# Kernel optimization log

Hardware: AMD Instinct MI355X
Metric: run time of the kernel (lower is better)

## Reference

```python
import jax, jax.numpy as jnp
import numpy as np

B, T0, H0, W0 = 8, 32, 16, 16
DV, DA, NH = 1024, 512, 16
L2 = 2048
EPS = 1e-6


def setup_inputs() -> dict:
    key = jax.random.key(0)
    ks = jax.random.split(key, 16)
    s = 0.02
    inp = {
        "video_x": jax.random.normal(ks[0], (B, T0 * H0 * W0, DV), jnp.float32),
        "audio_x": jax.random.normal(ks[1], (B, L2, DA), jnp.float32),
        "probe": jax.random.normal(ks[2], (1, 1, DV), jnp.float32) * s,
        "wq": jax.random.normal(ks[3], (DV, DV), jnp.float32) * s,
        "wk": jax.random.normal(ks[4], (DV, DV), jnp.float32) * s,
        "wv": jax.random.normal(ks[5], (DV, DV), jnp.float32) * s,
        "bq": jnp.zeros((DV,), jnp.float32),
        "bk": jnp.zeros((DV,), jnp.float32),
        "bv": jnp.zeros((DV,), jnp.float32),
        "wo": jax.random.normal(ks[6], (DV, DV), jnp.float32) * s,
        "bo": jnp.zeros((DV,), jnp.float32),
        "ln_g": jnp.ones((DV,), jnp.float32),
        "ln_b": jnp.zeros((DV,), jnp.float32),
        "proj_w": jax.random.normal(ks[7], (DA, DV), jnp.float32) * s,
        "proj_b": jnp.zeros((DA,), jnp.float32),
        "logit_scale": jnp.array([3.0], jnp.float32),
        "logit_bias": jnp.array([-3.9], jnp.float32),
        "T": T0, "H": H0, "W": W0,
    }
    return inp


def reference(video_x, audio_x, probe, wq, wk, wv, bq, bk, bv, wo, bo,
              ln_g, ln_b, proj_w, proj_b, logit_scale, logit_bias, T, H, W):
    Bv, L1, D = video_x.shape
    S = H * W
    dh = D // NH
    x = video_x.reshape(Bv, T, S, D)
    # single probe query, shared across B*T: project once
    q = (probe[0, 0] @ wq.T + bq).reshape(NH, dh)                      # [h,dh]
    k = (jnp.einsum('btsd,ed->btse', x, wk) + bk).reshape(Bv, T, S, NH, dh)
    v = (jnp.einsum('btsd,ed->btse', x, wv) + bv).reshape(Bv, T, S, NH, dh)
    scores = jnp.einsum('hd,btshd->bthcaptured'[:0] or 0, k) if False else jnp.einsum('hd,btshd->btsh', q, k) / jnp.sqrt(jnp.float32(dh))
    attn = jax.nn.softmax(scores, axis=2)                              # over S
    ctx = jnp.einsum('btsh,btshd->bthd', attn, v).reshape(Bv, T, D)
    pooled = ctx @ wo.T + bo                                           # [B,T,D]
    # LayerNorm
    mu = pooled.mean(-1, keepdims=True)
    var = ((pooled - mu) ** 2).mean(-1, keepdims=True)
    pooled = (pooled - mu) / jnp.sqrt(var + EPS) * ln_g + ln_b
    # project to audio dim, L2-normalize both sides
    vt = pooled @ proj_w.T + proj_b                                    # [B,T,Da]
    vt = vt / jnp.linalg.norm(vt, axis=-1, keepdims=True)
    a = audio_x / jnp.linalg.norm(audio_x, axis=-1, keepdims=True)
    sim = jnp.einsum('btd,bld->btl', vt, a)
    return sim * jnp.exp(logit_scale[0]) + logit_bias[0]
```

## Files before the change

kernel.cpp:

```cpp
#include <hip/hip_runtime.h>


#define FB_QWT    0u
#define FB_QB     16384u
#define FB_QF     16400u
#define FB_CTXX   18432u
#define FB_CTXP   4212736u
#define FB_POOLP  4737024u
#define FB_LNO    5261312u
#define FB_VTP    5523456u
#define FB_FLOATS 5785600u

typedef __attribute__((ext_vector_type(8))) short short8v;
typedef __attribute__((ext_vector_type(4))) float float4v;

__device__ __forceinline__ void bar_lds() {
    asm volatile("s_waitcnt lgkmcnt(0)\n\ts_barrier" ::: "memory");
}

__global__ __launch_bounds__(256) void k_qflat(const float* __restrict__ probe,
                                               const float* __restrict__ wq,
                                               const float* __restrict__ bq,
                                               float* __restrict__ qf) {
    int e = blockIdx.x, tid = threadIdx.x;
    const float* wr = wq + (size_t)e * 1024;
    float s = 0.f;
    for (int k = tid; k < 1024; k += 256) s += probe[k] * wr[k];
    s += __shfl_xor(s, 1);  s += __shfl_xor(s, 2);  s += __shfl_xor(s, 4);
    s += __shfl_xor(s, 8);  s += __shfl_xor(s, 16); s += __shfl_xor(s, 32);
    __shared__ float sm[4];
    if ((tid & 63) == 0) sm[tid >> 6] = s;
    __syncthreads();
    if (tid == 0) qf[e] = sm[0] + sm[1] + sm[2] + sm[3] + bq[e];
}

__global__ __launch_bounds__(64) void k_qwt(const float* __restrict__ qf,
                                            const float* __restrict__ wk,
                                            const float* __restrict__ bk,
                                            float* __restrict__ qwt_hd,
                                            float* __restrict__ qbs) {
    int kc = blockIdx.x, h = blockIdx.y, tid = threadIdx.x;
    int d = kc * 64 + tid;
    float s = 0.f;
    for (int e0 = 0; e0 < 64; ++e0) {
        int e = h * 64 + e0;
        s += qf[e] * wk[(size_t)e * 1024 + d];
    }
    qwt_hd[h * 1024 + d] = s * 0.125f;
    if (kc == 0) {
        float p = qf[h * 64 + tid] * bk[h * 64 + tid];
        p += __shfl_xor(p, 1);  p += __shfl_xor(p, 2);  p += __shfl_xor(p, 4);
        p += __shfl_xor(p, 8);  p += __shfl_xor(p, 16); p += __shfl_xor(p, 32);
        if (tid == 0) qbs[h] = p * 0.125f;
    }
}

__device__ __forceinline__ unsigned bf_rne(float f) {
    unsigned u = __float_as_uint(f);
    return (u + 0x7FFFu + ((u >> 16) & 1u)) >> 16;
}
__device__ __forceinline__ uint2 pack_bf4(float4 v) {
    uint2 r;
    r.x = bf_rne(v.x) | (bf_rne(v.y) << 16);
    r.y = bf_rne(v.z) | (bf_rne(v.w) << 16);
    return r;
}

__global__ __launch_bounds__(512, 2) void k1_attn(const float* __restrict__ x,
                                                  const float* __restrict__ qwt_hd,
                                                  const float* __restrict__ qbs,
                                                  float* __restrict__ ctxx) {
    __shared__ __align__(16) unsigned short xbf[16][1056];
    __shared__ __align__(16) unsigned short qwbf[16][1056];
    __shared__ __align__(16) float part[8][16][16];
    __shared__ __align__(16) float p_lds[16][16];
    __shared__ float qb_lds[16];
    __shared__ float linv_lds[16];

    const int tid  = threadIdx.x;
    const int lane = tid & 63;
    const int w    = tid >> 6;
    const int hq   = tid >> 7;
    const int cc   = tid & 127;
    const int bt   = blockIdx.x;
    const float* xb = x + (size_t)bt * 262144;

#pragma unroll
    for (int i = 0; i < 8; ++i) {
        int f4i = tid + i * 512;
        int hr = f4i >> 8, col4 = f4i & 255;
        float4 v = *(const float4*)(qwt_hd + hr * 1024 + col4 * 4);
        *(uint2*)&qwbf[hr][col4 * 4] = pack_bf4(v);
    }
    if (tid < 16) qb_lds[tid] = qbs[tid];

    float lacc = 0.f;
    float4 acc[8];
#pragma unroll
    for (int i = 0; i < 8; ++i) acc[i] = make_float4(0.f, 0.f, 0.f, 0.f);

    float4 st[8];
#pragma unroll
    for (int i = 0; i < 8; ++i)
        st[i] = *(const float4*)(xb + (size_t)(tid + i * 512) * 4);

    for (int c = 0; c < 16; ++c) {
        bar_lds();
#pragma unroll
        for (int i = 0; i < 8; ++i) {
            int f4i = tid + i * 512;
            int r = f4i >> 8, col4 = f4i & 255;
            *(uint2*)&xbf[r][col4 * 4] = pack_bf4(st[i]);
        }
        if (c < 15) {
            const float* nb = xb + (size_t)(c + 1) * 16384;
#pragma unroll
            for (int i = 0; i < 8; ++i)
                st[i] = *(const float4*)(nb + (size_t)(tid + i * 512) * 4);
        }
        bar_lds();
        {
            const int row = lane & 15;
            const int g   = lane >> 4;
            float4v cfr = {0.f, 0.f, 0.f, 0.f};
#pragma unroll
            for (int ks = 0; ks < 4; ++ks) {
                const int koff = (w * 4 + ks) * 32 + g * 8;
                short8v afr = *(const short8v*)&xbf[row][koff];
                short8v bfr = *(const short8v*)&qwbf[row][koff];
                cfr = __builtin_amdgcn_mfma_f32_16x16x32_bf16(afr, bfr, cfr, 0, 0, 0);
            }
#pragma unroll
            for (int r2 = 0; r2 < 4; ++r2)
                part[w][(lane >> 4) * 4 + r2][lane & 15] = cfr[r2];
        }
        bar_lds();
        if (tid < 256) {
            int s = tid >> 4, h = tid & 15;
            float sc = 0.f;
#pragma unroll
            for (int pw = 0; pw < 8; ++pw) sc += part[pw][s][h];
            p_lds[s][h] = __expf(sc + qb_lds[h]);
        }
        bar_lds();
        if (tid < 16) {
            float ll = 0.f;
#pragma unroll
            for (int s = 0; s < 16; ++s) ll += p_lds[s][tid];
            lacc += ll;
        }
#pragma unroll
        for (int r = 0; r < 16; ++r) {
            uint4 xv = *(const uint4*)&xbf[r][cc * 8];
            float x0 = __uint_as_float(xv.x << 16);
            float x1 = __uint_as_float(xv.x & 0xFFFF0000u);
            float x2 = __uint_as_float(xv.y << 16);
            float x3 = __uint_as_float(xv.y & 0xFFFF0000u);
            float x4 = __uint_as_float(xv.z << 16);
            float x5 = __uint_as_float(xv.z & 0xFFFF0000u);
            float x6 = __uint_as_float(xv.w << 16);
            float x7 = __uint_as_float(xv.w & 0xFFFF0000u);
            float4 p4 = *(const float4*)&p_lds[r][hq * 4];
            acc[0].x += p4.x * x0; acc[0].y += p4.x * x1; acc[0].z += p4.x * x2; acc[0].w += p4.x * x3;
            acc[1].x += p4.y * x0; acc[1].y += p4.y * x1; acc[1].z += p4.y * x2; acc[1].w += p4.y * x3;
            acc[2].x += p4.z * x0; acc[2].y += p4.z * x1; acc[2].z += p4.z * x2; acc[2].w += p4.z * x3;
            acc[3].x += p4.w * x0; acc[3].y += p4.w * x1; acc[3].z += p4.w * x2; acc[3].w += p4.w * x3;
            acc[4].x += p4.x * x4; acc[4].y += p4.x * x5; acc[4].z += p4.x * x6; acc[4].w += p4.x * x7;
            acc[5].x += p4.y * x4; acc[5].y += p4.y * x5; acc[5].z += p4.y * x6; acc[5].w += p4.y * x7;
            acc[6].x += p4.z * x4; acc[6].y += p4.z * x5; acc[6].z += p4.z * x6; acc[6].w += p4.z * x7;
            acc[7].x += p4.w * x4; acc[7].y += p4.w * x5; acc[7].z += p4.w * x6; acc[7].w += p4.w * x7;
        }
    }

    bar_lds();
    if (tid < 16) linv_lds[tid] = 1.0f / lacc;
    bar_lds();
    float* ob = ctxx + (size_t)bt * 16384;
#pragma unroll
    for (int i = 0; i < 4; ++i) {
        float li = linv_lds[hq * 4 + i];
        float4 o0 = acc[i];
        float4 o1 = acc[4 + i];
        o0.x *= li; o0.y *= li; o0.z *= li; o0.w *= li;
        o1.x *= li; o1.y *= li; o1.z *= li; o1.w *= li;
        float* dst = ob + (hq * 4 + i) * 1024 + cc * 8;
        *(float4*)dst = o0;
        *(float4*)(dst + 4) = o1;
    }
}

template<int FOLD>
__global__ __launch_bounds__(256, 2) void k_gemm2(const float* __restrict__ A0,
                                                  const float* __restrict__ A1,
                                                  const float* __restrict__ biask,
                                                  const float* __restrict__ Bw,
                                                  float* __restrict__ outp,
                                                  unsigned a_rstride, unsigned a_cstride,
                                                  unsigned ostride) {
    __shared__ __align__(16) float a_s[16][68];
    __shared__ __align__(16) float b_s[64][68];
    const int tid = threadIdx.x;
    const int rc = blockIdx.x;
    const int cb = blockIdx.y;
    const int ks = blockIdx.z;
    const int koff = ks * 512;
    const int rr = tid >> 4;
    const int ee = tid & 15;

    const size_t abase = (size_t)(rc * 16 + rr) * a_rstride + (size_t)cb * a_cstride + koff;

    float ac0 = 0.f, ac1 = 0.f, ac2 = 0.f, ac3 = 0.f;

    for (int kc = 0; kc < 8; ++kc) {
        __syncthreads();
        {
            float4 av = *(const float4*)(A0 + abase + kc * 64 + ee * 4);
            if (FOLD == 1) {
                float4 a1v = *(const float4*)(A1 + abase + kc * 64 + ee * 4);
                float4 bk4 = *(const float4*)(biask + koff + kc * 64 + ee * 4);
                av.x += a1v.x + bk4.x; av.y += a1v.y + bk4.y;
                av.z += a1v.z + bk4.z; av.w += a1v.w + bk4.w;
            }
            *(float4*)&a_s[rr][ee * 4] = av;
        }
#pragma unroll
        for (int i = 0; i < 4; ++i) {
            int f4i = tid + i * 256;
            int e = f4i >> 4, k4 = f4i & 15;
            float4 bv4 = *(const float4*)(Bw + (size_t)(cb * 64 + e) * 1024 + koff + kc * 64 + k4 * 4);
            int cs = (k4 + (e >> 2)) & 15;
            *(float4*)&b_s[e][cs * 4] = bv4;
        }
        __syncthreads();
#pragma unroll
        for (int k4 = 0; k4 < 16; ++k4) {
            float4 av = *(const float4*)&a_s[rr][k4 * 4];
            int cs = (k4 + ee) & 15;
            float4 b0 = *(const float4*)&b_s[ee * 4 + 0][cs * 4];
            float4 b1 = *(const float4*)&b_s[ee * 4 + 1][cs * 4];
            float4 b2 = *(const float4*)&b_s[ee * 4 + 2][cs * 4];
            float4 b3 = *(const float4*)&b_s[ee * 4 + 3][cs * 4];
            ac0 += av.x * b0.x + av.y * b0.y + av.z * b0.z + av.w * b0.w;
            ac1 += av.x * b1.x + av.y * b1.y + av.z * b1.z + av.w * b1.w;
            ac2 += av.x * b2.x + av.y * b2.y + av.z * b2.z + av.w * b2.w;
            ac3 += av.x * b3.x + av.y * b3.y + av.z * b3.z + av.w * b3.w;
        }
    }
    float4 o = make_float4(ac0, ac1, ac2, ac3);
    *(float4*)(outp + (size_t)ks * 256 * ostride + (size_t)(rc * 16 + rr) * ostride + cb * 64 + ee * 4) = o;
}

__global__ __launch_bounds__(256) void k_ln(const float* __restrict__ poolp,
                                            const float* __restrict__ bo,
                                            const float* __restrict__ g,
                                            const float* __restrict__ bb,
                                            float* __restrict__ out) {
    __shared__ float sm[8];
    int row = blockIdx.x, tid = threadIdx.x;
    float4 v0 = *(const float4*)(poolp + (size_t)row * 1024 + tid * 4);
    float4 v1 = *(const float4*)(poolp + 262144u + (size_t)row * 1024 + tid * 4);
    float4 bv = *(const float4*)(bo + tid * 4);
    float4 v;
    v.x = v0.x + v1.x + bv.x; v.y = v0.y + v1.y + bv.y;
    v.z = v0.z + v1.z + bv.z; v.w = v0.w + v1.w + bv.w;
    float s = v.x + v.y + v.z + v.w;
    float q = v.x * v.x + v.y * v.y + v.z * v.z + v.w * v.w;
    s += __shfl_xor(s, 1);  q += __shfl_xor(q, 1);
    s += __shfl_xor(s, 2);  q += __shfl_xor(q, 2);
    s += __shfl_xor(s, 4);  q += __shfl_xor(q, 4);
    s += __shfl_xor(s, 8);  q += __shfl_xor(q, 8);
    s += __shfl_xor(s, 16); q += __shfl_xor(q, 16);
    s += __shfl_xor(s, 32); q += __shfl_xor(q, 32);
    if ((tid & 63) == 0) { sm[tid >> 6] = s; sm[4 + (tid >> 6)] = q; }
    __syncthreads();
    float S = sm[0] + sm[1] + sm[2] + sm[3];
    float Q = sm[4] + sm[5] + sm[6] + sm[7];
    float mu = S * (1.f / 1024.f);
    float var = Q * (1.f / 1024.f) - mu * mu;
    float rs = rsqrtf(var + 1e-6f);
    float4 gg = *(const float4*)(g + tid * 4);
    float4 be = *(const float4*)(bb + tid * 4);
    float4 o;
    o.x = (v.x - mu) * rs * gg.x + be.x;
    o.y = (v.y - mu) * rs * gg.y + be.y;
    o.z = (v.z - mu) * rs * gg.z + be.z;
    o.w = (v.w - mu) * rs * gg.w + be.w;
    *(float4*)(out + (size_t)row * 1024 + tid * 4) = o;
}

__global__ __launch_bounds__(256, 2) void k_sim(const float* __restrict__ vtp,
                                                const float* __restrict__ pb,
                                                const float* __restrict__ audio,
                                                const float* __restrict__ ls,
                                                const float* __restrict__ lb,
                                                float* __restrict__ out) {
    __shared__ float a_s[64][65];
    __shared__ float v_s[32][65];
    __shared__ float rinv_a[64];
    __shared__ float rinv_v[32];
    const int tid = threadIdx.x;
    const int lc = blockIdx.x;
    const int b  = blockIdx.y;
    const int al = tid >> 2, ak = (tid & 3) * 16;
    const int vl = tid >> 3, vk = (tid & 7) * 8;
    const int rg = tid >> 4, lg = tid & 15;
    float ssa = 0.f, ssv = 0.f;
    float c00=0,c01=0,c02=0,c03=0,c10=0,c11=0,c12=0,c13=0;

    for (int kc = 0; kc < 8; ++kc) {
        __syncthreads();
        {
            const float* ap = audio + (size_t)b * 1048576 + (size_t)(lc * 64 + al) * 512 + kc * 64 + ak;
#pragma unroll
            for (int i = 0; i < 4; ++i) {
                float4 wv4 = *(const float4*)(ap + i * 4);
                ssa += wv4.x * wv4.x + wv4.y * wv4.y + wv4.z * wv4.z + wv4.w * wv4.w;
                a_s[al][ak + i * 4 + 0] = wv4.x; a_s[al][ak + i * 4 + 1] = wv4.y;
                a_s[al][ak + i * 4 + 2] = wv4.z; a_s[al][ak + i * 4 + 3] = wv4.w;
            }
            const size_t voff = (size_t)(b * 32 + vl) * 512 + kc * 64 + vk;
#pragma unroll
            for (int i = 0; i < 2; ++i) {
                float4 p0 = *(const float4*)(vtp + voff + i * 4);
                float4 p1 = *(const float4*)(vtp + 131072u + voff + i * 4);
                float4 pbv = *(const float4*)(pb + kc * 64 + vk + i * 4);
                float4 wv4;
                wv4.x = p0.x + p1.x + pbv.x; wv4.y = p0.y + p1.y + pbv.y;
                wv4.z = p0.z + p1.z + pbv.z; wv4.w = p0.w + p1.w + pbv.w;
                ssv += wv4.x * wv4.x + wv4.y * wv4.y + wv4.z * wv4.z + wv4.w * wv4.w;
                v_s[vl][vk + i * 4 + 0] = wv4.x; v_s[vl][vk + i * 4 + 1] = wv4.y;
                v_s[vl][vk + i * 4 + 2] = wv4.z; v_s[vl][vk + i * 4 + 3] = wv4.w;
            }
        }
        __syncthreads();
#pragma unroll 2
        for (int k = 0; k < 64; ++k) {
            float v0 = v_s[rg * 2 + 0][k];
            float v1 = v_s[rg * 2 + 1][k];
            float x0 = a_s[lg * 4 + 0][k];
            float x1 = a_s[lg * 4 + 1][k];
            float x2 = a_s[lg * 4 + 2][k];
            float x3 = a_s[lg * 4 + 3][k];
            c00 += v0 * x0; c01 += v0 * x1; c02 += v0 * x2; c03 += v0 * x3;
            c10 += v1 * x0; c11 += v1 * x1; c12 += v1 * x2; c13 += v1 * x3;
        }
    }
    ssa += __shfl_xor(ssa, 1); ssa += __shfl_xor(ssa, 2);
    if ((tid & 3) == 0) rinv_a[al] = rsqrtf(ssa);
    ssv += __shfl_xor(ssv, 1); ssv += __shfl_xor(ssv, 2); ssv += __shfl_xor(ssv, 4);
    if ((tid & 7) == 0) rinv_v[vl] = rsqrtf(ssv);
    __syncthreads();
    const float sc = __expf(ls[0]);
    const float bias = lb[0];
    float ra0 = rinv_a[lg * 4 + 0], ra1 = rinv_a[lg * 4 + 1];
    float ra2 = rinv_a[lg * 4 + 2], ra3 = rinv_a[lg * 4 + 3];
    float accs[2][4] = {{c00,c01,c02,c03},{c10,c11,c12,c13}};
#pragma unroll
    for (int cr = 0; cr < 2; ++cr) {
        int t = rg * 2 + cr;
        float rv = rinv_v[t] * sc;
        float4 o;
        o.x = accs[cr][0] * rv * ra0 + bias;
        o.y = accs[cr][1] * rv * ra1 + bias;
        o.z = accs[cr][2] * rv * ra2 + bias;
        o.w = accs[cr][3] * rv * ra3 + bias;
        *(float4*)(out + (size_t)b * 65536 + (size_t)t * 2048 + lc * 64 + lg * 4) = o;
    }
}

extern "C" void kernel_launch(void* const* d_in, const int* in_sizes, int n_in,
                              void* d_out, int out_size, void* d_ws, size_t ws_size,
                              hipStream_t stream) {
    (void)in_sizes; (void)n_in; (void)out_size;
    const float* video = (const float*)d_in[0];
    const float* audio = (const float*)d_in[1];
    const float* probe = (const float*)d_in[2];
    const float* wq    = (const float*)d_in[3];
    const float* wk    = (const float*)d_in[4];
    const float* wv    = (const float*)d_in[5];
    const float* bq    = (const float*)d_in[6];
    const float* bk    = (const float*)d_in[7];
    const float* bv    = (const float*)d_in[8];
    const float* wo    = (const float*)d_in[9];
    const float* bo    = (const float*)d_in[10];
    const float* lng   = (const float*)d_in[11];
    const float* lnb   = (const float*)d_in[12];
    const float* pw    = (const float*)d_in[13];
    const float* pb    = (const float*)d_in[14];
    const float* ls    = (const float*)d_in[15];
    const float* lb    = (const float*)d_in[16];
    float* ws  = (float*)d_ws;
    float* out = (float*)d_out;
    if (ws_size < FB_FLOATS * sizeof(float)) return;

    float* qwt  = ws + FB_QWT;
    float* qbs  = ws + FB_QB;
    float* qf   = ws + FB_QF;
    float* ctxx = ws + FB_CTXX;
    float* ctxp = ws + FB_CTXP;
    float* poolp= ws + FB_POOLP;
    float* lno  = ws + FB_LNO;
    float* vtp  = ws + FB_VTP;

    k_qflat<<<dim3(1024), dim3(256), 0, stream>>>(probe, wq, bq, qf);
    k_qwt<<<dim3(16, 16), dim3(64), 0, stream>>>(qf, wk, bk, qwt, qbs);
    k1_attn<<<dim3(256), dim3(512), 0, stream>>>(video, qwt, qbs, ctxx);
    k_gemm2<0><<<dim3(16, 16, 2), dim3(256), 0, stream>>>(ctxx, nullptr, nullptr, wv, ctxp,
                                                          16384u, 1024u, 1024u);
    k_gemm2<1><<<dim3(16, 16, 2), dim3(256), 0, stream>>>(ctxp, ctxp + 262144u, bv, wo, poolp,
                                                          1024u, 0u, 1024u);
    k_ln<<<dim3(256), dim3(256), 0, stream>>>(poolp, bo, lng, lnb, lno);
    k_gemm2<0><<<dim3(16, 8, 2), dim3(256), 0, stream>>>(lno, nullptr, nullptr, pw, vtp,
                                                         1024u, 0u, 512u);
    k_sim<<<dim3(32, 8), dim3(256), 0, stream>>>(vtp, pb, audio, ls, lb, out);
}
```

Before: 173.4 us.

## Fuse query prep kernels, swizzle LDS tiles, store context in bf16

Merges the two probe-query preparation kernels into a single 16-block kernel that keeps the projected query in shared memory, removing one launch and a global round trip. Applies an XOR swizzle to the bf16 x and query tiles in LDS to cut bank conflicts on the MFMA fragment and context reads. Writes the attention context as bf16 instead of fp32 and has the next GEMM read bf16, halving that intermediate traffic at the cost of extra rounding. The fused prep kernel runs on only 16 blocks, which may leave it latency bound.

```diff
diff --git a/kernel.cpp b/kernel.cpp
--- a/kernel.cpp
+++ b/kernel.cpp
@@ -18,37 +18,42 @@
     asm volatile("s_waitcnt lgkmcnt(0)\n\ts_barrier" ::: "memory");
 }
 
-__global__ __launch_bounds__(256) void k_qflat(const float* __restrict__ probe,
+#define SW(R, C) ((C) ^ (((R) & 7) << 3))
+
+__global__ __launch_bounds__(256) void k_qprep(const float* __restrict__ probe,
                                                const float* __restrict__ wq,
                                                const float* __restrict__ bq,
-                                               float* __restrict__ qf) {
-    int e = blockIdx.x, tid = threadIdx.x;
-    const float* wr = wq + (size_t)e * 1024;
-    float s = 0.f;
-    for (int k = tid; k < 1024; k += 256) s += probe[k] * wr[k];
-    s += __shfl_xor(s, 1);  s += __shfl_xor(s, 2);  s += __shfl_xor(s, 4);
-    s += __shfl_xor(s, 8);  s += __shfl_xor(s, 16); s += __shfl_xor(s, 32);
-    __shared__ float sm[4];
-    if ((tid & 63) == 0) sm[tid >> 6] = s;
+                                               const float* __restrict__ wk,
+                                               const float* __restrict__ bk,
+                                               float* __restrict__ qwt_hd,
+                                               float* __restrict__ qbs) {
+    __shared__ float qf_s[64];
+    const int h = blockIdx.x, tid = threadIdx.x;
+    {
+        const int e0 = tid >> 2, part = tid & 3;
+        const int e = h * 64 + e0;
+        const float* wr = wq + (size_t)e * 1024 + part * 256;
+        const float* pr = probe + part * 256;
+        float s = 0.f;
+        for (int k = 0; k < 256; k += 4) {
+            float4 a = *(const float4*)(pr + k);
+            float4 b = *(const float4*)(wr + k);
+            s += a.x * b.x + a.y * b.y + a.z * b.z + a.w * b.w;
+        }
+        s += __shfl_xor(s, 1); s += __shfl_xor(s, 2);
+        if (part == 0) qf_s[e0] = s + bq[e];
+    }
     __syncthreads();
-    if (tid == 0) qf[e] = sm[0] + sm[1] + sm[2] + sm[3] + bq[e];
-}
-
-__global__ __launch_bounds__(64) void k_qwt(const float* __restrict__ qf,
-                                            const float* __restrict__ wk,
-                                            const float* __restrict__ bk,
-                                            float* __restrict__ qwt_hd,
-                                            float* __restrict__ qbs) {
-    int kc = blockIdx.x, h = blockIdx.y, tid = threadIdx.x;
-    int d = kc * 64 + tid;
-    float s = 0.f;
-    for (int e0 = 0; e0 < 64; ++e0) {
-        int e = h * 64 + e0;
-        s += qf[e] * wk[(size_t)e * 1024 + d];
-    }
-    qwt_hd[h * 1024 + d] = s * 0.125f;
-    if (kc == 0) {
-        float p = qf[h * 64 + tid] * bk[h * 64 + tid];
+#pragma unroll
+    for (int i = 0; i < 4; ++i) {
+        int d = tid + i * 256;
+        float s = 0.f;
+        for (int e0 = 0; e0 < 64; ++e0)
+            s += qf_s[e0] * wk[(size_t)(h * 64 + e0) * 1024 + d];
+        qwt_hd[h * 1024 + d] = s * 0.125f;
+    }
+    if (tid < 64) {
+        float p = qf_s[tid] * bk[h * 64 + tid];
         p += __shfl_xor(p, 1);  p += __shfl_xor(p, 2);  p += __shfl_xor(p, 4);
         p += __shfl_xor(p, 8);  p += __shfl_xor(p, 16); p += __shfl_xor(p, 32);
         if (tid == 0) qbs[h] = p * 0.125f;
@@ -90,7 +95,7 @@
         int f4i = tid + i * 512;
         int hr = f4i >> 8, col4 = f4i & 255;
         float4 v = *(const float4*)(qwt_hd + hr * 1024 + col4 * 4);
-        *(uint2*)&qwbf[hr][col4 * 4] = pack_bf4(v);
+        *(uint2*)&qwbf[hr][SW(hr, col4 * 4)] = pack_bf4(v);
     }
     if (tid < 16) qb_lds[tid] = qbs[tid];
 
@@ -110,7 +115,7 @@
         for (int i = 0; i < 8; ++i) {
             int f4i = tid + i * 512;
             int r = f4i >> 8, col4 = f4i & 255;
-            *(uint2*)&xbf[r][col4 * 4] = pack_bf4(st[i]);
+            *(uint2*)&xbf[r][SW(r, col4 * 4)] = pack_bf4(st[i]);
         }
         if (c < 15) {
             const float* nb = xb + (size_t)(c + 1) * 16384;
@@ -126,8 +131,8 @@
 #pragma unroll
             for (int ks = 0; ks < 4; ++ks) {
                 const int koff = (w * 4 + ks) * 32 + g * 8;
-                short8v afr = *(const short8v*)&xbf[row][koff];
-                short8v bfr = *(const short8v*)&qwbf[row][koff];
+                short8v afr = *(const short8v*)&xbf[row][SW(row, koff)];
+                short8v bfr = *(const short8v*)&qwbf[row][SW(row, koff)];
                 cfr = __builtin_amdgcn_mfma_f32_16x16x32_bf16(afr, bfr, cfr, 0, 0, 0);
             }
 #pragma unroll
@@ -151,7 +156,7 @@
         }
 #pragma unroll
         for (int r = 0; r < 16; ++r) {
-            uint4 xv = *(const uint4*)&xbf[r][cc * 8];
+            uint4 xv = *(const uint4*)&xbf[r][SW(r, cc * 8)];
             float x0 = __uint_as_float(xv.x << 16);
             float x1 = __uint_as_float(xv.x & 0xFFFF0000u);
             float x2 = __uint_as_float(xv.y << 16);
@@ -175,7 +180,7 @@
     bar_lds();
     if (tid < 16) linv_lds[tid] = 1.0f / lacc;
     bar_lds();
-    float* ob = ctxx + (size_t)bt * 16384;
+    unsigned short* ob = (unsigned short*)ctxx + (size_t)bt * 16384;
 #pragma unroll
     for (int i = 0; i < 4; ++i) {
         float li = linv_lds[hq * 4 + i];
@@ -183,13 +188,14 @@
         float4 o1 = acc[4 + i];
         o0.x *= li; o0.y *= li; o0.z *= li; o0.w *= li;
         o1.x *= li; o1.y *= li; o1.z *= li; o1.w *= li;
-        float* dst = ob + (hq * 4 + i) * 1024 + cc * 8;
-        *(float4*)dst = o0;
-        *(float4*)(dst + 4) = o1;
-    }
-}
-
-template<int FOLD>
+        uint2 p0 = pack_bf4(o0);
+        uint2 p1 = pack_bf4(o1);
+        uint4 pk = make_uint4(p0.x, p0.y, p1.x, p1.y);
+        *(uint4*)(ob + (hq * 4 + i) * 1024 + cc * 8) = pk;
+    }
+}
+
+template<int FOLD, int ABF16>
 __global__ __launch_bounds__(256, 2) void k_gemm2(const float* __restrict__ A0,
                                                   const float* __restrict__ A1,
                                                   const float* __restrict__ biask,
@@ -214,7 +220,17 @@
     for (int kc = 0; kc < 8; ++kc) {
         __syncthreads();
         {
-            float4 av = *(const float4*)(A0 + abase + kc * 64 + ee * 4);
+            float4 av;
+            if (ABF16) {
+                const unsigned short* A0h = (const unsigned short*)A0;
+                uint2 u = *(const uint2*)(A0h + abase + kc * 64 + ee * 4);
+                av.x = __uint_as_float(u.x << 16);
+                av.y = __uint_as_float(u.x & 0xFFFF0000u);
+                av.z = __uint_as_float(u.y << 16);
+                av.w = __uint_as_float(u.y & 0xFFFF0000u);
+            } else {
+                av = *(const float4*)(A0 + abase + kc * 64 + ee * 4);
+            }
             if (FOLD == 1) {
                 float4 a1v = *(const float4*)(A1 + abase + kc * 64 + ee * 4);
                 float4 bk4 = *(const float4*)(biask + koff + kc * 64 + ee * 4);
@@ -395,22 +411,20 @@
 
     float* qwt  = ws + FB_QWT;
     float* qbs  = ws + FB_QB;
-    float* qf   = ws + FB_QF;
     float* ctxx = ws + FB_CTXX;
     float* ctxp = ws + FB_CTXP;
     float* poolp= ws + FB_POOLP;
     float* lno  = ws + FB_LNO;
     float* vtp  = ws + FB_VTP;
 
-    k_qflat<<<dim3(1024), dim3(256), 0, stream>>>(probe, wq, bq, qf);
-    k_qwt<<<dim3(16, 16), dim3(64), 0, stream>>>(qf, wk, bk, qwt, qbs);
+    k_qprep<<<dim3(16), dim3(256), 0, stream>>>(probe, wq, bq, wk, bk, qwt, qbs);
     k1_attn<<<dim3(256), dim3(512), 0, stream>>>(video, qwt, qbs, ctxx);
-    k_gemm2<0><<<dim3(16, 16, 2), dim3(256), 0, stream>>>(ctxx, nullptr, nullptr, wv, ctxp,
-                                                          16384u, 1024u, 1024u);
-    k_gemm2<1><<<dim3(16, 16, 2), dim3(256), 0, stream>>>(ctxp, ctxp + 262144u, bv, wo, poolp,
-                                                          1024u, 0u, 1024u);
+    k_gemm2<0, 1><<<dim3(16, 16, 2), dim3(256), 0, stream>>>(ctxx, nullptr, nullptr, wv, ctxp,
+                                                             16384u, 1024u, 1024u);
+    k_gemm2<1, 0><<<dim3(16, 16, 2), dim3(256), 0, stream>>>(ctxp, ctxp + 262144u, bv, wo, poolp,
+                                                             1024u, 0u, 1024u);
     k_ln<<<dim3(256), dim3(256), 0, stream>>>(poolp, bo, lng, lnb, lno);
-    k_gemm2<0><<<dim3(16, 8, 2), dim3(256), 0, stream>>>(lno, nullptr, nullptr, pw, vtp,
-                                                         1024u, 0u, 512u);
+    k_gemm2<0, 0><<<dim3(16, 8, 2), dim3(256), 0, stream>>>(lno, nullptr, nullptr, pw, vtp,
+                                                            1024u, 0u, 512u);
     k_sim<<<dim3(32, 8), dim3(256), 0, stream>>>(vtp, pb, audio, ls, lb, out);
 }
```

New measurement: 230.3 us. +32.8%, slower.
